# Kernel tuning notes

Hardware: AMD Instinct MI355X
Metric: run time of the kernel (lower is better)

## Reference

```python
import jax, jax.numpy as jnp
import numpy as np
from jax import lax

WIN_SIZE = 11
SIGMA = 1.5
K1, K2 = 0.01, 0.03
DATA_RANGE = 1.0


def _gauss_1d(size=WIN_SIZE, sigma=SIGMA):
    coords = jnp.arange(size, dtype=jnp.float32) - size // 2
    g = jnp.exp(-(coords ** 2) / (2.0 * sigma ** 2))
    return g / jnp.sum(g)


def _blur(x, win):
    # x: (1, C, H, W); separable depthwise gaussian, VALID padding (pytorch_msssim)
    C = x.shape[1]
    dn = ('NCHW', 'OIHW', 'NCHW')
    kw = jnp.tile(win.reshape(1, 1, 1, -1), (C, 1, 1, 1))  # (C,1,1,K)
    kh = jnp.tile(win.reshape(1, 1, -1, 1), (C, 1, 1, 1))  # (C,1,K,1)
    x = lax.conv_general_dilated(x, kw, (1, 1), 'VALID',
                                 dimension_numbers=dn, feature_group_count=C)
    x = lax.conv_general_dilated(x, kh, (1, 1), 'VALID',
                                 dimension_numbers=dn, feature_group_count=C)
    return x


def _ssim_loss(pred, targ, height, width):
    x = pred.reshape(1, 3, height, width)
    y = targ.reshape(1, 3, height, width)
    win = _gauss_1d()
    C1 = (K1 * DATA_RANGE) ** 2
    C2 = (K2 * DATA_RANGE) ** 2

    mu1 = _blur(x, win)
    mu2 = _blur(y, win)
    mu1_sq = mu1 * mu1
    mu2_sq = mu2 * mu2
    mu1_mu2 = mu1 * mu2
    sigma1_sq = _blur(x * x, win) - mu1_sq
    sigma2_sq = _blur(y * y, win) - mu2_sq
    sigma12 = _blur(x * y, win) - mu1_mu2

    cs_map = (2.0 * sigma12 + C2) / (sigma1_sq + sigma2_sq + C2)
    ssim_map = ((2.0 * mu1_mu2 + C1) / (mu1_sq + mu2_sq + C1)) * cs_map
    return 1.0 - jnp.mean(ssim_map)


def setup_inputs() -> dict:
    key = jax.random.key(0)
    k1, k2 = jax.random.split(key)
    H, W = 2048, 2048
    return {
        'predicted_img': jax.random.uniform(k1, (1, 3, H, W), dtype=jnp.float32),
        'target_img': jax.random.uniform(k2, (1, 3, H, W), dtype=jnp.float32),
        'height': H,
        'width': W,
    }


def reference(predicted_img, target_img, height, width):
    return _ssim_loss(predicted_img, target_img, height, width)
```

## Files before the change

### kernel.cpp

```cpp
#include <hip/hip_runtime.h>
#include <math.h>

typedef float f32x2 __attribute__((ext_vector_type(2)));
typedef float f32x4 __attribute__((ext_vector_type(4)));

#define HH    2048
#define WW    2048
#define NCH   3
#define NOUT  2038
#define OWID  64
#define OH    128
#define CROWS 16
#define BUF   32
#define SWP   76
#define HAW   66
#define HCW   68
#define NTX   32
#define NTY   16
#define NBLOCKS (NTX*NTY*NCH)
#define NOUT_TOTAL 12460332.0f

__device__ __forceinline__ float ssim_term(float mu1, float mu2,
                                           float b11, float b22, float b12) {
    const float c1v = 1e-4f, c2v = 9e-4f;
    float mu1sq = mu1 * mu1;
    float mu2sq = mu2 * mu2;
    float mu12  = mu1 * mu2;
    float s11 = b11 - mu1sq;
    float s22 = b22 - mu2sq;
    float s12 = b12 - mu12;
    float csn = 2.f * s12 + c2v;
    float csd = s11 + s22 + c2v;
    float ln  = 2.f * mu12 + c1v;
    float ld  = mu1sq + mu2sq + c1v;
    return (csn * ln) * __builtin_amdgcn_rcpf(csd * ld);
}

__global__ __launch_bounds__(256, 2)
void ssim_main(const float* __restrict__ x, const float* __restrict__ y,
               float* __restrict__ partials) {
    __shared__ f32x2 sxy[CROWS][SWP];
    __shared__ f32x2 hbA[BUF][HAW];
    __shared__ f32x2 hbB[BUF][HAW];
    __shared__ float hbC[BUF][HCW];
    __shared__ float wsum[4];

    const int tid = threadIdx.x;
    const int gx0 = blockIdx.x * OWID;
    const int gy0 = blockIdx.y * OH;
    const float* xb = x + (size_t)blockIdx.z * HH * WW;
    const float* yb = y + (size_t)blockIdx.z * HH * WW;

    float w[11];
    {
        float s = 0.f;
        #pragma unroll
        for (int i = 0; i < 11; ++i) {
            float d = (float)(i - 5);
            w[i] = expf(-d * d / 4.5f);
            s += w[i];
        }
        float inv = 1.f / s;
        #pragma unroll
        for (int i = 0; i < 11; ++i) w[i] *= inv;
    }

    auto loadA = [&](int base) {
        for (int u = tid; u < CROWS * 19; u += 256) {
            int lr = u / 19;
            int c0 = (u - lr * 19) * 4;
            int gy = gy0 + base + lr; if (gy > HH - 1) gy = HH - 1;
            const float* xr = xb + (size_t)gy * WW;
            const float* yr = yb + (size_t)gy * WW;
            int gxc = gx0 + c0;
            float4 xf, yf;
            if (gxc + 4 <= WW) {
                xf = *(const float4*)(xr + gxc);
                yf = *(const float4*)(yr + gxc);
            } else {
                int g0 = gxc     < WW ? gxc     : WW - 1;
                int g1 = gxc + 1 < WW ? gxc + 1 : WW - 1;
                int g2 = gxc + 2 < WW ? gxc + 2 : WW - 1;
                int g3 = gxc + 3 < WW ? gxc + 3 : WW - 1;
                xf = make_float4(xr[g0], xr[g1], xr[g2], xr[g3]);
                yf = make_float4(yr[g0], yr[g1], yr[g2], yr[g3]);
            }
            *(f32x4*)&sxy[lr][c0]     = (f32x4){xf.x, yf.x, xf.y, yf.y};
            *(f32x4*)&sxy[lr][c0 + 2] = (f32x4){xf.z, yf.z, xf.w, yf.w};
        }
    };

    auto blurB = [&](int base) {
        int lr = tid >> 4;
        int c0 = (tid & 15) * 4;
        int slot = (base + lr) & (BUF - 1);
        f32x2 p[16];
        #pragma unroll
        for (int t = 0; t < 8; ++t) {
            f32x4 raw = *(const f32x4*)&sxy[lr][c0 + 2 * t];
            p[2 * t]     = (f32x2){raw.x, raw.y};
            p[2 * t + 1] = (f32x2){raw.z, raw.w};
        }
        f32x2 q[14]; float pr[14];
        #pragma unroll
        for (int t = 0; t < 14; ++t) {
            q[t]  = p[t] * p[t];
            pr[t] = p[t].x * p[t].y;
        }
        f32x2 hA[4] = {}, hB[4] = {};
        float hC[4] = {};
        #pragma unroll
        for (int k = 0; k < 11; ++k) {
            f32x2 wk2 = (f32x2){w[k], w[k]};
            #pragma unroll
            for (int j = 0; j < 4; ++j) {
                hA[j] = __builtin_elementwise_fma(wk2, p[j + k], hA[j]);
                hB[j] = __builtin_elementwise_fma(wk2, q[j + k], hB[j]);
                hC[j] = fmaf(w[k], pr[j + k], hC[j]);
            }
        }
        *(f32x4*)&hbA[slot][c0]     = (f32x4){hA[0].x, hA[0].y, hA[1].x, hA[1].y};
        *(f32x4*)&hbA[slot][c0 + 2] = (f32x4){hA[2].x, hA[2].y, hA[3].x, hA[3].y};
        *(f32x4*)&hbB[slot][c0]     = (f32x4){hB[0].x, hB[0].y, hB[1].x, hB[1].y};
        *(f32x4*)&hbB[slot][c0 + 2] = (f32x4){hB[2].x, hB[2].y, hB[3].x, hB[3].y};
        *(float4*)&hbC[slot][c0]    = make_float4(hC[0], hC[1], hC[2], hC[3]);
    };

    float partial = 0.f;

    loadA(0);  __syncthreads(); blurB(0);  __syncthreads();
    loadA(16); __syncthreads(); blurB(16); __syncthreads();

    for (int m = 0; m < 8; ++m) {
        const int o0 = m * CROWS;
        {
            const int col = tid & 63;
            const int r0  = o0 + (tid >> 6) * 4;
            f32x2 vA[14], vB[14]; float vC[14];
            #pragma unroll
            for (int j = 0; j < 14; ++j) {
                int slot = (r0 + j) & (BUF - 1);
                vA[j] = hbA[slot][col];
                vB[j] = hbB[slot][col];
                vC[j] = hbC[slot][col];
            }
            const int ocol = gx0 + col;
            #pragma unroll
            for (int i = 0; i < 4; ++i) {
                f32x2 aA = {0.f, 0.f}, aB = {0.f, 0.f};
                float aC = 0.f;
                #pragma unroll
                for (int k = 0; k < 11; ++k) {
                    f32x2 wk2 = (f32x2){w[k], w[k]};
                    aA = __builtin_elementwise_fma(wk2, vA[i + k], aA);
                    aB = __builtin_elementwise_fma(wk2, vB[i + k], aB);
                    aC = fmaf(w[k], vC[i + k], aC);
                }
                int orow = gy0 + r0 + i;
                if (orow < NOUT && ocol < NOUT)
                    partial += ssim_term(aA.x, aA.y, aB.x, aB.y, aC);
            }
        }
        __syncthreads();
        if (m < 7) {
            loadA(32 + o0); __syncthreads();
            blurB(32 + o0); __syncthreads();
        }
    }

    #pragma unroll
    for (int off = 32; off > 0; off >>= 1)
        partial += __shfl_down(partial, off, 64);
    if ((tid & 63) == 0) wsum[tid >> 6] = partial;
    __syncthreads();
    if (tid == 0) {
        int bid = (blockIdx.z * gridDim.y + blockIdx.y) * gridDim.x + blockIdx.x;
        partials[bid] = wsum[0] + wsum[1] + wsum[2] + wsum[3];
    }
}

__global__ __launch_bounds__(256)
void ssim_finalize(const float* __restrict__ partials, float* __restrict__ out) {
    __shared__ float ws[4];
    float s = 0.f;
    for (int i = threadIdx.x; i < NBLOCKS / 4; i += 256) {
        float4 v = ((const float4*)partials)[i];
        s += (v.x + v.y) + (v.z + v.w);
    }
    #pragma unroll
    for (int off = 32; off > 0; off >>= 1)
        s += __shfl_down(s, off, 64);
    if ((threadIdx.x & 63) == 0) ws[threadIdx.x >> 6] = s;
    __syncthreads();
    if (threadIdx.x == 0)
        out[0] = 1.f - (ws[0] + ws[1] + ws[2] + ws[3]) / NOUT_TOTAL;
}

extern "C" void kernel_launch(void* const* d_in, const int* in_sizes, int n_in,
                              void* d_out, int out_size, void* d_ws, size_t ws_size,
                              hipStream_t stream) {
    const float* x = (const float*)d_in[0];
    const float* y = (const float*)d_in[1];
    float* out = (float*)d_out;
    float* partials = (float*)d_ws;

    dim3 grid(NTX, NTY, NCH);
    ssim_main<<<grid, dim3(256), 0, stream>>>(x, y, partials);
    ssim_finalize<<<1, 256, 0, stream>>>(partials, out);
}
```

Before: 180.7 us.

## Load rows directly into registers and prefetch next tile during vertical pass

Removes the shared staging buffer for raw x/y rows: each thread loads its 14-column window straight from global memory into registers and blurs it horizontally. The next row group's global loads are issued before the vertical pass so their latency overlaps that compute, and one barrier per iteration is dropped. The ring buffer shrinks from 32 to 28 rows, using modulo indexing, and the vertical pass streams rows while accumulating four outputs. This adds redundant overlapping global loads per thread and more register pressure.

```diff
diff --git a/kernel.cpp b/kernel.cpp
--- a/kernel.cpp
+++ b/kernel.cpp
@@ -11,8 +11,7 @@
 #define OWID  64
 #define OH    128
 #define CROWS 16
-#define BUF   32
-#define SWP   76
+#define BUF   28
 #define HAW   66
 #define HCW   68
 #define NTX   32
@@ -39,7 +38,6 @@
 __global__ __launch_bounds__(256, 2)
 void ssim_main(const float* __restrict__ x, const float* __restrict__ y,
                float* __restrict__ partials) {
-    __shared__ f32x2 sxy[CROWS][SWP];
     __shared__ f32x2 hbA[BUF][HAW];
     __shared__ f32x2 hbB[BUF][HAW];
     __shared__ float hbC[BUF][HCW];
@@ -65,42 +63,56 @@
         for (int i = 0; i < 11; ++i) w[i] *= inv;
     }
 
-    auto loadA = [&](int base) {
-        for (int u = tid; u < CROWS * 19; u += 256) {
-            int lr = u / 19;
-            int c0 = (u - lr * 19) * 4;
-            int gy = gy0 + base + lr; if (gy > HH - 1) gy = HH - 1;
-            const float* xr = xb + (size_t)gy * WW;
-            const float* yr = yb + (size_t)gy * WW;
-            int gxc = gx0 + c0;
-            float4 xf, yf;
-            if (gxc + 4 <= WW) {
-                xf = *(const float4*)(xr + gxc);
-                yf = *(const float4*)(yr + gxc);
+    const int lr  = tid >> 4;
+    const int c0  = (tid & 15) * 4;
+    const int gxc = gx0 + c0;
+
+    f32x4 px[3], py[3];
+    f32x2 px3, py3;
+
+    auto PF = [&](int base) {
+        int gy = gy0 + base + lr; if (gy > HH - 1) gy = HH - 1;
+        const float* xr = xb + (size_t)gy * WW;
+        const float* yr = yb + (size_t)gy * WW;
+        #pragma unroll
+        for (int a = 0; a < 3; ++a) {
+            int g = gxc + 4 * a;
+            if (g + 4 <= WW) {
+                px[a] = *(const f32x4*)(xr + g);
+                py[a] = *(const f32x4*)(yr + g);
             } else {
-                int g0 = gxc     < WW ? gxc     : WW - 1;
-                int g1 = gxc + 1 < WW ? gxc + 1 : WW - 1;
-                int g2 = gxc + 2 < WW ? gxc + 2 : WW - 1;
-                int g3 = gxc + 3 < WW ? gxc + 3 : WW - 1;
-                xf = make_float4(xr[g0], xr[g1], xr[g2], xr[g3]);
-                yf = make_float4(yr[g0], yr[g1], yr[g2], yr[g3]);
-            }
-            *(f32x4*)&sxy[lr][c0]     = (f32x4){xf.x, yf.x, xf.y, yf.y};
-            *(f32x4*)&sxy[lr][c0 + 2] = (f32x4){xf.z, yf.z, xf.w, yf.w};
+                int g0 = g     < WW ? g     : WW - 1;
+                int g1 = g + 1 < WW ? g + 1 : WW - 1;
+                int g2 = g + 2 < WW ? g + 2 : WW - 1;
+                int g3 = g + 3 < WW ? g + 3 : WW - 1;
+                px[a] = (f32x4){xr[g0], xr[g1], xr[g2], xr[g3]};
+                py[a] = (f32x4){yr[g0], yr[g1], yr[g2], yr[g3]};
+            }
+        }
+        {
+            int g = gxc + 12;
+            if (g + 2 <= WW) {
+                px3 = *(const f32x2*)(xr + g);
+                py3 = *(const f32x2*)(yr + g);
+            } else {
+                int g0 = g     < WW ? g     : WW - 1;
+                int g1 = g + 1 < WW ? g + 1 : WW - 1;
+                px3 = (f32x2){xr[g0], xr[g1]};
+                py3 = (f32x2){yr[g0], yr[g1]};
+            }
         }
     };
 
-    auto blurB = [&](int base) {
-        int lr = tid >> 4;
-        int c0 = (tid & 15) * 4;
-        int slot = (base + lr) & (BUF - 1);
-        f32x2 p[16];
-        #pragma unroll
-        for (int t = 0; t < 8; ++t) {
-            f32x4 raw = *(const f32x4*)&sxy[lr][c0 + 2 * t];
-            p[2 * t]     = (f32x2){raw.x, raw.y};
-            p[2 * t + 1] = (f32x2){raw.z, raw.w};
-        }
+    auto BLUR = [&](int base, bool tailMask) {
+        int slot = (base + lr) % BUF;
+        f32x2 p[14];
+        #pragma unroll
+        for (int a = 0; a < 3; ++a)
+            #pragma unroll
+            for (int i = 0; i < 4; ++i)
+                p[4 * a + i] = (f32x2){px[a][i], py[a][i]};
+        p[12] = (f32x2){px3.x, py3.x};
+        p[13] = (f32x2){px3.y, py3.y};
         f32x2 q[14]; float pr[14];
         #pragma unroll
         for (int t = 0; t < 14; ++t) {
@@ -119,52 +131,60 @@
                 hC[j] = fmaf(w[k], pr[j + k], hC[j]);
             }
         }
-        *(f32x4*)&hbA[slot][c0]     = (f32x4){hA[0].x, hA[0].y, hA[1].x, hA[1].y};
-        *(f32x4*)&hbA[slot][c0 + 2] = (f32x4){hA[2].x, hA[2].y, hA[3].x, hA[3].y};
-        *(f32x4*)&hbB[slot][c0]     = (f32x4){hB[0].x, hB[0].y, hB[1].x, hB[1].y};
-        *(f32x4*)&hbB[slot][c0 + 2] = (f32x4){hB[2].x, hB[2].y, hB[3].x, hB[3].y};
-        *(float4*)&hbC[slot][c0]    = make_float4(hC[0], hC[1], hC[2], hC[3]);
+        if (!tailMask || lr < 10) {
+            *(f32x4*)&hbA[slot][c0]     = (f32x4){hA[0].x, hA[0].y, hA[1].x, hA[1].y};
+            *(f32x4*)&hbA[slot][c0 + 2] = (f32x4){hA[2].x, hA[2].y, hA[3].x, hA[3].y};
+            *(f32x4*)&hbB[slot][c0]     = (f32x4){hB[0].x, hB[0].y, hB[1].x, hB[1].y};
+            *(f32x4*)&hbB[slot][c0 + 2] = (f32x4){hB[2].x, hB[2].y, hB[3].x, hB[3].y};
+            *(float4*)&hbC[slot][c0]    = make_float4(hC[0], hC[1], hC[2], hC[3]);
+        }
     };
 
     float partial = 0.f;
 
-    loadA(0);  __syncthreads(); blurB(0);  __syncthreads();
-    loadA(16); __syncthreads(); blurB(16); __syncthreads();
+    PF(0);  BLUR(0, false);
+    PF(16); BLUR(16, true);
+    __syncthreads();
+
+    const int col  = tid & 63;
+    const int wid  = tid >> 6;
+    const int ocol = gx0 + col;
 
     for (int m = 0; m < 8; ++m) {
-        const int o0 = m * CROWS;
+        if (m < 7) PF(16 * m + 26);
         {
-            const int col = tid & 63;
-            const int r0  = o0 + (tid >> 6) * 4;
-            f32x2 vA[14], vB[14]; float vC[14];
+            const int r0 = 16 * m + wid * 4;
+            int s = r0 % BUF;
+            f32x2 aA[4] = {}, aB[4] = {};
+            float aC[4] = {};
             #pragma unroll
             for (int j = 0; j < 14; ++j) {
-                int slot = (r0 + j) & (BUF - 1);
-                vA[j] = hbA[slot][col];
-                vB[j] = hbB[slot][col];
-                vC[j] = hbC[slot][col];
-            }
-            const int ocol = gx0 + col;
+                f32x2 va = hbA[s][col];
+                f32x2 vb = hbB[s][col];
+                float vc = hbC[s][col];
+                #pragma unroll
+                for (int i = 0; i < 4; ++i) {
+                    const int k = j - i;
+                    if (k >= 0 && k < 11) {
+                        f32x2 wk2 = (f32x2){w[k], w[k]};
+                        aA[i] = __builtin_elementwise_fma(wk2, va, aA[i]);
+                        aB[i] = __builtin_elementwise_fma(wk2, vb, aB[i]);
+                        aC[i] = fmaf(w[k], vc, aC[i]);
+                    }
+                }
+                s = (s == BUF - 1) ? 0 : s + 1;
+            }
             #pragma unroll
             for (int i = 0; i < 4; ++i) {
-                f32x2 aA = {0.f, 0.f}, aB = {0.f, 0.f};
-                float aC = 0.f;
-                #pragma unroll
-                for (int k = 0; k < 11; ++k) {
-                    f32x2 wk2 = (f32x2){w[k], w[k]};
-                    aA = __builtin_elementwise_fma(wk2, vA[i + k], aA);
-                    aB = __builtin_elementwise_fma(wk2, vB[i + k], aB);
-                    aC = fmaf(w[k], vC[i + k], aC);
-                }
                 int orow = gy0 + r0 + i;
                 if (orow < NOUT && ocol < NOUT)
-                    partial += ssim_term(aA.x, aA.y, aB.x, aB.y, aC);
+                    partial += ssim_term(aA[i].x, aA[i].y, aB[i].x, aB[i].y, aC[i]);
             }
         }
         __syncthreads();
         if (m < 7) {
-            loadA(32 + o0); __syncthreads();
-            blurB(32 + o0); __syncthreads();
+            BLUR(16 * m + 26, false);
+            __syncthreads();
         }
     }
 
```

Result: faster. 162.5 us (-10.1%).
